# Kernel tuning notes

Measured on AMD Instinct MI355X. Metric: run time of the kernel, lower is better.

The kernel has to match this reference:

```python
import jax, jax.numpy as jnp
import numpy as np

B, S, D = 4, 4096, 128

def setup_inputs() -> dict:
    key = jax.random.key(0)
    kq, kk, kv = jax.random.split(key, 3)
    q = jax.random.normal(kq, (B, S, D), dtype=jnp.float32)
    k = jax.random.normal(kk, (B, S, D), dtype=jnp.float32)
    v = jax.random.normal(kv, (B, S, D), dtype=jnp.float32)
    return {"q": q, "k": k, "v": v}

def reference(q, k, v):
    d_model = q.shape[-1]
    scale = 1.0 / jnp.sqrt(jnp.asarray(d_model, q.dtype))
    # [B, S, S] scores
    scores = jnp.einsum('bqd,bkd->bqk', q, k) * scale
    s = q.shape[1]
    causal = jnp.tril(jnp.ones((s, s), dtype=bool))
    neg_inf = jnp.asarray(-jnp.inf, scores.dtype)
    scores = jnp.where(causal[None, :, :], scores, neg_inf)
    attn = jax.nn.softmax(scores, axis=-1)
    return jnp.einsum('bqk,bkd->bqd', attn, v)
```

## Files before the change

kernel.cpp:

```cpp
#include <hip/hip_runtime.h>


#define B_   4
#define S_   4096
#define D_   128
#define BN   64
#define NT_  64
#define QT_  32
#define RMAX 4
#define BLOB_SHORTS 16384
#define MASKVAL (-1.0e30f)

typedef __attribute__((ext_vector_type(8))) short bf16x8;
typedef __attribute__((ext_vector_type(4))) float f32x4;

__device__ __forceinline__ short f2bf(float x) {
    unsigned u = __builtin_bit_cast(unsigned, x);
    unsigned r = (u + 0x7fffu + ((u >> 16) & 1u)) >> 16;
    return (short)r;
}
__device__ __forceinline__ float ex2(float x) { return __builtin_amdgcn_exp2f(x); }
__device__ __forceinline__ unsigned pkbf(float lo, float hi) {
    return (unsigned)(unsigned short)f2bf(lo) | ((unsigned)(unsigned short)f2bf(hi) << 16);
}
__device__ __forceinline__ void gl_lds16(const short* g, short* l) {
    __builtin_amdgcn_global_load_lds(
        (const __attribute__((address_space(1))) unsigned int*)g,
        (__attribute__((address_space(3))) unsigned int*)l, 16, 0, 0);
}

__global__ __launch_bounds__(256) void prep(const float* __restrict__ Qg,
                                            const float* __restrict__ Kg,
                                            const float* __restrict__ Vg,
                                            short* __restrict__ Qbf,
                                            short* __restrict__ KV)
{
    __shared__ short vt[64][40];
    const int id  = blockIdx.x;
    const int tid = threadIdx.x;
    const float SC = 0.12751740f;

    if (id < 1024) {
        const int b = id & 3, tile = (id >> 2) & 63, q4 = id >> 8;
        const int n = q4 * 16 + (tid >> 4);
        const int G = tid & 15;
        const size_t rowoff = ((size_t)b * S_ + (size_t)tile * 64 + n) * D_ + G * 8;
        short* blob = KV + (size_t)(b * NT_ + tile) * BLOB_SHORTS;
        {
            float4 a = *reinterpret_cast<const float4*>(Qg + rowoff);
            float4 c = *reinterpret_cast<const float4*>(Qg + rowoff + 4);
            bf16x8 v;
            v[0] = f2bf(a.x * SC); v[1] = f2bf(a.y * SC); v[2] = f2bf(a.z * SC); v[3] = f2bf(a.w * SC);
            v[4] = f2bf(c.x * SC); v[5] = f2bf(c.y * SC); v[6] = f2bf(c.z * SC); v[7] = f2bf(c.w * SC);
            *reinterpret_cast<bf16x8*>(Qbf + rowoff) = v;
        }
        {
            float4 a = *reinterpret_cast<const float4*>(Kg + rowoff);
            float4 c = *reinterpret_cast<const float4*>(Kg + rowoff + 4);
            bf16x8 v;
            v[0] = f2bf(a.x); v[1] = f2bf(a.y); v[2] = f2bf(a.z); v[3] = f2bf(a.w);
            v[4] = f2bf(c.x); v[5] = f2bf(c.y); v[6] = f2bf(c.z); v[7] = f2bf(c.w);
            const int p = (G & 8) | ((G & 7) ^ (n & 7));
            *reinterpret_cast<bf16x8*>(blob + n * 128 + p * 8) = v;
        }
    } else {
        const int u = id - 1024;
        const int b = u & 3, tile = (u >> 2) & 63, dq = u >> 8;
        short* blob = KV + (size_t)(b * NT_ + tile) * BLOB_SHORTS;
        {
            const int n = tid >> 2, c8 = tid & 3;
            const size_t off = ((size_t)b * S_ + (size_t)tile * 64 + n) * D_ + dq * 32 + c8 * 8;
            float4 a = *reinterpret_cast<const float4*>(Vg + off);
            float4 c = *reinterpret_cast<const float4*>(Vg + off + 4);
            bf16x8 v;
            v[0] = f2bf(a.x); v[1] = f2bf(a.y); v[2] = f2bf(a.z); v[3] = f2bf(a.w);
            v[4] = f2bf(c.x); v[5] = f2bf(c.y); v[6] = f2bf(c.z); v[7] = f2bf(c.w);
            *reinterpret_cast<bf16x8*>(&vt[n][c8 * 8]) = v;
        }
        __syncthreads();
        {
            const int dl = tid >> 3, G = tid & 7;
            const int d  = dq * 32 + dl;
            bf16x8 g;
#pragma unroll
            for (int i = 0; i < 8; ++i) g[i] = vt[G * 8 + i][dl];
            const int p = G ^ (d & 7);
            *reinterpret_cast<bf16x8*>(blob + 8192 + d * 64 + p * 8) = g;
        }
    }
}

template<bool SPLIT>
__global__ __launch_bounds__(512, 4) void fa_fwd(const short* __restrict__ Qbf,
                                                 const short* __restrict__ KV,
                                                 float* __restrict__ Og,
                                                 float* __restrict__ Op,
                                                 float* __restrict__ Ml,
                                                 int R)
{
    __shared__ short lkv[2][BLOB_SHORTS];

    const int tid  = threadIdx.x;
    const int wv   = tid >> 6;
    const int lane = tid & 63;
    const int m    = lane & 15;
    const int quad = lane >> 4;
    const int m7   = m & 7;

    int batch, t, lo, hi, chunk_id;
    {
        const int id = blockIdx.x;
        batch = id & 3;
        if (SPLIT) {
            int u = id >> 2;
            int tt = u / R;
            int r  = u - tt * R;
            t  = QT_ - 1 - tt;
            const int nk = 2 * t + 2;
            lo = r * nk / R;
            hi = (r + 1) * nk / R;
            chunk_id = (batch * QT_ + t) * R + r;
            if (lo >= hi) return;
        } else {
            t  = QT_ - 1 - (id >> 2);
            lo = 0; hi = 2 * t + 2; chunk_id = 0;
        }
    }

    bf16x8 qf[4];
    {
        const short* qp = Qbf + ((size_t)batch * S_ + (size_t)t * 128 + wv * 16 + m) * D_ + quad * 8;
#pragma unroll
        for (int c = 0; c < 4; ++c)
            qf[c] = *reinterpret_cast<const bf16x8*>(qp + c * 32);
    }

    f32x4 acc[8];
#pragma unroll
    for (int i = 0; i < 8; ++i) acc[i] = (f32x4){0.f, 0.f, 0.f, 0.f};
    float mrun = MASKVAL, lrun = 0.f;

    const size_t tilebase = (size_t)batch * NT_ * BLOB_SHORTS;
#define STAGE(KT, BUF) do {                                                   \
        const short* g_ = KV + tilebase + (size_t)(KT) * BLOB_SHORTS + tid * 8;\
        short* l_ = (BUF) + tid * 8;                                          \
        _Pragma("unroll")                                                     \
        for (int c_ = 0; c_ < 4; ++c_)                                        \
            gl_lds16(g_ + c_ * 4096, l_ + c_ * 4096);                         \
    } while (0)

    STAGE(lo, lkv[0]);

    for (int kt = lo; kt < hi; ++kt) {
        const short* cur = lkv[(kt - lo) & 1];
        short* nxt = lkv[(kt - lo + 1) & 1];
        __syncthreads();
        if (kt + 1 < hi) STAGE(kt + 1, nxt);

        const short* lk = cur;
        const short* lv = cur + 8192;

        f32x4 st[4];
#pragma unroll
        for (int nt = 0; nt < 4; ++nt) st[nt] = (f32x4){0.f, 0.f, 0.f, 0.f};
#pragma unroll
        for (int c = 0; c < 4; ++c) {
            const int p = ((c >> 1) * 8) | ((((c & 1) * 4) | quad) ^ m7);
#pragma unroll
            for (int nt = 0; nt < 4; ++nt) {
                bf16x8 kf = *reinterpret_cast<const bf16x8*>(lk + nt * 2048 + m * 128 + p * 8);
                st[nt] = __builtin_amdgcn_mfma_f32_16x16x32_bf16(kf, qf[c], st[nt], 0, 0, 0);
            }
        }

        if (kt >= 2 * t) {
            const int kbase = (kt - 2 * t) * 64;
            const int qloc  = wv * 16 + m;
#pragma unroll
            for (int nt = 0; nt < 4; ++nt)
#pragma unroll
                for (int r = 0; r < 4; ++r)
                    if (kbase + nt * 16 + quad * 4 + r > qloc) st[nt][r] = MASKVAL;
        }

        float mx = MASKVAL;
#pragma unroll
        for (int nt = 0; nt < 4; ++nt)
#pragma unroll
            for (int r = 0; r < 4; ++r) mx = fmaxf(mx, st[nt][r]);
        mx = fmaxf(mx, __shfl_xor(mx, 16));
        mx = fmaxf(mx, __shfl_xor(mx, 32));
        const float mnew = fmaxf(mrun, mx);
        const float al   = ex2(mrun - mnew);
        mrun = mnew;
        float sum = 0.f;
#pragma unroll
        for (int nt = 0; nt < 4; ++nt)
#pragma unroll
            for (int r = 0; r < 4; ++r) {
                float pv = ex2(st[nt][r] - mnew);
                st[nt][r] = pv;
                sum += pv;
            }
        sum += __shfl_xor(sum, 16);
        sum += __shfl_xor(sum, 32);
        lrun = lrun * al + sum;
#pragma unroll
        for (int r = 0; r < 4; ++r) {
            float alq = __shfl(al, quad * 4 + r);
#pragma unroll
            for (int ct = 0; ct < 8; ++ct) acc[ct][r] *= alq;
        }

        const int srcA = ((quad & 1) << 5) + m;
        const int srcB = srcA + 16;
        const bool loq = quad < 2;
#pragma unroll
        for (int ks = 0; ks < 2; ++ks) {
            unsigned pk0 = pkbf(st[2 * ks][0],     st[2 * ks][1]);
            unsigned pk1 = pkbf(st[2 * ks][2],     st[2 * ks][3]);
            unsigned pk2 = pkbf(st[2 * ks + 1][0], st[2 * ks + 1][1]);
            unsigned pk3 = pkbf(st[2 * ks + 1][2], st[2 * ks + 1][3]);
            unsigned w0a = __shfl((int)pk0, srcA);
            unsigned w0b = __shfl((int)pk2, srcA);
            unsigned w1a = __shfl((int)pk1, srcA);
            unsigned w1b = __shfl((int)pk3, srcA);
            unsigned w2a = __shfl((int)pk0, srcB);
            unsigned w2b = __shfl((int)pk2, srcB);
            unsigned w3a = __shfl((int)pk1, srcB);
            unsigned w3b = __shfl((int)pk3, srcB);
            int4 wi;
            wi.x = (int)(loq ? w0a : w0b);
            wi.y = (int)(loq ? w1a : w1b);
            wi.z = (int)(loq ? w2a : w2b);
            wi.w = (int)(loq ? w3a : w3b);
            bf16x8 pf = __builtin_bit_cast(bf16x8, wi);
            const int p = (ks * 4 + quad) ^ m7;
#pragma unroll
            for (int ct = 0; ct < 8; ++ct) {
                bf16x8 vf = *reinterpret_cast<const bf16x8*>(lv + ct * 1024 + m * 64 + p * 8);
                acc[ct] = __builtin_amdgcn_mfma_f32_16x16x32_bf16(pf, vf, acc[ct], 0, 0, 0);
            }
        }
    }
#undef STAGE

    const int row0 = wv * 16 + quad * 4;
    if (SPLIT) {
        float* ob = Op + (size_t)chunk_id * (128 * D_);
#pragma unroll
        for (int r = 0; r < 4; ++r)
#pragma unroll
            for (int ct = 0; ct < 8; ++ct)
                ob[(row0 + r) * D_ + ct * 16 + m] = acc[ct][r];
        if (lane < 16) {
            float* mlb = Ml + (size_t)chunk_id * (128 * 2) + (wv * 16 + lane) * 2;
            mlb[0] = mrun;
            mlb[1] = lrun;
        }
    } else {
        const float inv = 1.0f / lrun;
        const size_t obase = ((size_t)batch * S_ + (size_t)t * 128 + row0) * D_;
#pragma unroll
        for (int r = 0; r < 4; ++r) {
            float invq = __shfl(inv, quad * 4 + r);
#pragma unroll
            for (int ct = 0; ct < 8; ++ct)
                Og[obase + (size_t)r * D_ + ct * 16 + m] = acc[ct][r] * invq;
        }
    }
}

template<int RR>
__global__ __launch_bounds__(256) void fa_merge(const float* __restrict__ Op,
                                                const float* __restrict__ Ml,
                                                float* __restrict__ Og)
{
    const int x   = blockIdx.x;
    const int btq = x >> 4;
    const int oct = x & 15;
    const int t   = btq & (QT_ - 1);
    const int nk  = 2 * t + 2;
    const int row = oct * 8 + (threadIdx.x >> 5);
    const int cg  = threadIdx.x & 31;
    const size_t cbase = (size_t)btq * RR;

    float mg = MASKVAL;
#pragma unroll
    for (int r = 0; r < RR; ++r) {
        int lo = r * nk / RR, hi = (r + 1) * nk / RR;
        if (lo < hi) mg = fmaxf(mg, Ml[(cbase + r) * (128 * 2) + row * 2]);
    }
    float l = 0.f;
    f32x4 a = (f32x4){0.f, 0.f, 0.f, 0.f};
#pragma unroll
    for (int r = 0; r < RR; ++r) {
        int lo = r * nk / RR, hi = (r + 1) * nk / RR;
        if (lo >= hi) continue;
        float mr = Ml[(cbase + r) * (128 * 2) + row * 2];
        float lr = Ml[(cbase + r) * (128 * 2) + row * 2 + 1];
        float w  = ex2(mr - mg);
        l += lr * w;
        a += w * *reinterpret_cast<const f32x4*>(Op + (cbase + r) * (128 * D_) + row * D_ + cg * 4);
    }
    *reinterpret_cast<f32x4*>(Og + (size_t)btq * (128 * D_) + row * D_ + cg * 4) = a * (1.0f / l);
}

extern "C" void kernel_launch(void* const* d_in, const int* in_sizes, int n_in,
                              void* d_out, int out_size, void* d_ws, size_t ws_size,
                              hipStream_t stream) {
    const float* q = (const float*)d_in[0];
    const float* k = (const float*)d_in[1];
    const float* v = (const float*)d_in[2];
    float* o = (float*)d_out;

    const size_t QBF_BYTES = (size_t)B_ * S_ * D_ * 2;
    const size_t KV_BYTES  = (size_t)B_ * NT_ * BLOB_SHORTS * 2;
    const size_t PREFIX    = QBF_BYTES + KV_BYTES;
    const size_t O_FLOATS  = (size_t)B_ * QT_ * 128 * D_;
    const size_t ML_FLOATS = (size_t)B_ * QT_ * 128 * 2;
    const size_t PER_R     = (O_FLOATS + ML_FLOATS) * sizeof(float);

    char* ws = (char*)d_ws;
    short* Qbf = (short*)ws;
    short* KV  = (short*)(ws + QBF_BYTES);

    int R = 0;
    if (ws_size > PREFIX) {
        R = (int)((ws_size - PREFIX) / PER_R);
        if (R > RMAX) R = RMAX;
    }

    prep<<<dim3(2048), 256, 0, stream>>>(q, k, v, Qbf, KV);

    if (R >= 1) {
        float* Op = (float*)(ws + PREFIX);
        float* Ml = Op + (size_t)R * O_FLOATS;
        fa_fwd<true><<<dim3(B_ * QT_ * R), 512, 0, stream>>>(Qbf, KV, nullptr, Op, Ml, R);
        switch (R) {
            case 1: fa_merge<1><<<dim3(B_ * QT_ * 16), 256, 0, stream>>>(Op, Ml, o); break;
            case 2: fa_merge<2><<<dim3(B_ * QT_ * 16), 256, 0, stream>>>(Op, Ml, o); break;
            case 3: fa_merge<3><<<dim3(B_ * QT_ * 16), 256, 0, stream>>>(Op, Ml, o); break;
            default: fa_merge<4><<<dim3(B_ * QT_ * 16), 256, 0, stream>>>(Op, Ml, o); break;
        }
    } else {
        fa_fwd<false><<<dim3(B_ * QT_), 512, 0, stream>>>(Qbf, KV, o, nullptr, nullptr, 1);
    }
}
```

Before: 123.5 us.

## Switch attention kernel to 32x32x16 MFMA with 4 waves of 32 rows

```diff
diff --git a/kernel.cpp b/kernel.cpp
--- a/kernel.cpp
+++ b/kernel.cpp
@@ -13,6 +13,7 @@
 
 typedef __attribute__((ext_vector_type(8))) short bf16x8;
 typedef __attribute__((ext_vector_type(4))) float f32x4;
+typedef __attribute__((ext_vector_type(16))) float f32x16;
 
 __device__ __forceinline__ short f2bf(float x) {
     unsigned u = __builtin_bit_cast(unsigned, x);
@@ -91,7 +92,7 @@
 }
 
 template<bool SPLIT>
-__global__ __launch_bounds__(512, 4) void fa_fwd(const short* __restrict__ Qbf,
+__global__ __launch_bounds__(256, 2) void fa_fwd(const short* __restrict__ Qbf,
                                                  const short* __restrict__ KV,
                                                  float* __restrict__ Og,
                                                  float* __restrict__ Op,
@@ -103,9 +104,9 @@
     const int tid  = threadIdx.x;
     const int wv   = tid >> 6;
     const int lane = tid & 63;
-    const int m    = lane & 15;
-    const int quad = lane >> 4;
-    const int m7   = m & 7;
+    const int col  = lane & 31;
+    const int half = lane >> 5;
+    const int c7   = col & 7;
 
     int batch, t, lo, hi, chunk_id;
     {
@@ -127,17 +128,19 @@
         }
     }
 
-    bf16x8 qf[4];
+    bf16x8 qf[8];
     {
-        const short* qp = Qbf + ((size_t)batch * S_ + (size_t)t * 128 + wv * 16 + m) * D_ + quad * 8;
-#pragma unroll
-        for (int c = 0; c < 4; ++c)
-            qf[c] = *reinterpret_cast<const bf16x8*>(qp + c * 32);
-    }
-
-    f32x4 acc[8];
-#pragma unroll
-    for (int i = 0; i < 8; ++i) acc[i] = (f32x4){0.f, 0.f, 0.f, 0.f};
+        const short* qp = Qbf + ((size_t)batch * S_ + (size_t)t * 128 + wv * 32 + col) * D_ + half * 8;
+#pragma unroll
+        for (int c = 0; c < 8; ++c)
+            qf[c] = *reinterpret_cast<const bf16x8*>(qp + c * 16);
+    }
+
+    f32x16 acc[4];
+#pragma unroll
+    for (int i = 0; i < 4; ++i)
+#pragma unroll
+        for (int r = 0; r < 16; ++r) acc[i][r] = 0.f;
     float mrun = MASKVAL, lrun = 0.f;
 
     const size_t tilebase = (size_t)batch * NT_ * BLOB_SHORTS;
@@ -145,8 +148,8 @@
         const short* g_ = KV + tilebase + (size_t)(KT) * BLOB_SHORTS + tid * 8;\
         short* l_ = (BUF) + tid * 8;                                          \
         _Pragma("unroll")                                                     \
-        for (int c_ = 0; c_ < 4; ++c_)                                        \
-            gl_lds16(g_ + c_ * 4096, l_ + c_ * 4096);                         \
+        for (int c_ = 0; c_ < 8; ++c_)                                        \
+            gl_lds16(g_ + c_ * 2048, l_ + c_ * 2048);                         \
     } while (0)
 
     STAGE(lo, lkv[0]);
@@ -160,114 +163,124 @@
         const short* lk = cur;
         const short* lv = cur + 8192;
 
-        f32x4 st[4];
-#pragma unroll
-        for (int nt = 0; nt < 4; ++nt) st[nt] = (f32x4){0.f, 0.f, 0.f, 0.f};
-#pragma unroll
-        for (int c = 0; c < 4; ++c) {
-            const int p = ((c >> 1) * 8) | ((((c & 1) * 4) | quad) ^ m7);
-#pragma unroll
-            for (int nt = 0; nt < 4; ++nt) {
-                bf16x8 kf = *reinterpret_cast<const bf16x8*>(lk + nt * 2048 + m * 128 + p * 8);
-                st[nt] = __builtin_amdgcn_mfma_f32_16x16x32_bf16(kf, qf[c], st[nt], 0, 0, 0);
+        f32x16 st[2];
+#pragma unroll
+        for (int i = 0; i < 2; ++i)
+#pragma unroll
+            for (int r = 0; r < 16; ++r) st[i][r] = 0.f;
+#pragma unroll
+        for (int c = 0; c < 8; ++c) {
+            const int G = 2 * c + half;
+            const int p = (G & 8) | ((G & 7) ^ c7);
+#pragma unroll
+            for (int kt32 = 0; kt32 < 2; ++kt32) {
+                const int n = kt32 * 32 + col;
+                bf16x8 kf = *reinterpret_cast<const bf16x8*>(lk + n * 128 + p * 8);
+                st[kt32] = __builtin_amdgcn_mfma_f32_32x32x16_bf16(kf, qf[c], st[kt32], 0, 0, 0);
             }
         }
 
         if (kt >= 2 * t) {
             const int kbase = (kt - 2 * t) * 64;
-            const int qloc  = wv * 16 + m;
-#pragma unroll
-            for (int nt = 0; nt < 4; ++nt)
-#pragma unroll
-                for (int r = 0; r < 4; ++r)
-                    if (kbase + nt * 16 + quad * 4 + r > qloc) st[nt][r] = MASKVAL;
+            const int qloc  = wv * 32 + col;
+#pragma unroll
+            for (int kt32 = 0; kt32 < 2; ++kt32)
+#pragma unroll
+                for (int r = 0; r < 16; ++r) {
+                    const int kl = kt32 * 32 + (r & 3) + 8 * (r >> 2) + 4 * half;
+                    if (kbase + kl > qloc) st[kt32][r] = MASKVAL;
+                }
         }
 
         float mx = MASKVAL;
 #pragma unroll
-        for (int nt = 0; nt < 4; ++nt)
-#pragma unroll
-            for (int r = 0; r < 4; ++r) mx = fmaxf(mx, st[nt][r]);
-        mx = fmaxf(mx, __shfl_xor(mx, 16));
+        for (int i = 0; i < 2; ++i)
+#pragma unroll
+            for (int r = 0; r < 16; ++r) mx = fmaxf(mx, st[i][r]);
         mx = fmaxf(mx, __shfl_xor(mx, 32));
         const float mnew = fmaxf(mrun, mx);
         const float al   = ex2(mrun - mnew);
         mrun = mnew;
         float sum = 0.f;
 #pragma unroll
-        for (int nt = 0; nt < 4; ++nt)
-#pragma unroll
-            for (int r = 0; r < 4; ++r) {
-                float pv = ex2(st[nt][r] - mnew);
-                st[nt][r] = pv;
+        for (int i = 0; i < 2; ++i)
+#pragma unroll
+            for (int r = 0; r < 16; ++r) {
+                float pv = ex2(st[i][r] - mnew);
+                st[i][r] = pv;
                 sum += pv;
             }
-        sum += __shfl_xor(sum, 16);
         sum += __shfl_xor(sum, 32);
         lrun = lrun * al + sum;
 #pragma unroll
-        for (int r = 0; r < 4; ++r) {
-            float alq = __shfl(al, quad * 4 + r);
-#pragma unroll
-            for (int ct = 0; ct < 8; ++ct) acc[ct][r] *= alq;
-        }
-
-        const int srcA = ((quad & 1) << 5) + m;
-        const int srcB = srcA + 16;
-        const bool loq = quad < 2;
-#pragma unroll
-        for (int ks = 0; ks < 2; ++ks) {
-            unsigned pk0 = pkbf(st[2 * ks][0],     st[2 * ks][1]);
-            unsigned pk1 = pkbf(st[2 * ks][2],     st[2 * ks][3]);
-            unsigned pk2 = pkbf(st[2 * ks + 1][0], st[2 * ks + 1][1]);
-            unsigned pk3 = pkbf(st[2 * ks + 1][2], st[2 * ks + 1][3]);
-            unsigned w0a = __shfl((int)pk0, srcA);
-            unsigned w0b = __shfl((int)pk2, srcA);
-            unsigned w1a = __shfl((int)pk1, srcA);
-            unsigned w1b = __shfl((int)pk3, srcA);
-            unsigned w2a = __shfl((int)pk0, srcB);
-            unsigned w2b = __shfl((int)pk2, srcB);
-            unsigned w3a = __shfl((int)pk1, srcB);
-            unsigned w3b = __shfl((int)pk3, srcB);
-            int4 wi;
-            wi.x = (int)(loq ? w0a : w0b);
-            wi.y = (int)(loq ? w1a : w1b);
-            wi.z = (int)(loq ? w2a : w2b);
-            wi.w = (int)(loq ? w3a : w3b);
-            bf16x8 pf = __builtin_bit_cast(bf16x8, wi);
-            const int p = (ks * 4 + quad) ^ m7;
-#pragma unroll
-            for (int ct = 0; ct < 8; ++ct) {
-                bf16x8 vf = *reinterpret_cast<const bf16x8*>(lv + ct * 1024 + m * 64 + p * 8);
-                acc[ct] = __builtin_amdgcn_mfma_f32_16x16x32_bf16(pf, vf, acc[ct], 0, 0, 0);
+        for (int i = 0; i < 4; ++i)
+#pragma unroll
+            for (int r = 0; r < 16; ++r) acc[i][r] *= al;
+
+#pragma unroll
+        for (int kt32 = 0; kt32 < 2; ++kt32) {
+            unsigned pw[4][2];
+#pragma unroll
+            for (int w = 0; w < 4; ++w) {
+                pw[w][0] = pkbf(st[kt32][4 * w],     st[kt32][4 * w + 1]);
+                pw[w][1] = pkbf(st[kt32][4 * w + 2], st[kt32][4 * w + 3]);
+            }
+#pragma unroll
+            for (int s1 = 0; s1 < 2; ++s1) {
+                unsigned snd0 = pw[2 * s1 + 1 - half][0];
+                unsigned snd1 = pw[2 * s1 + 1 - half][1];
+                unsigned rcv0 = __shfl_xor((int)snd0, 32);
+                unsigned rcv1 = __shfl_xor((int)snd1, 32);
+                unsigned own0 = pw[2 * s1 + half][0];
+                unsigned own1 = pw[2 * s1 + half][1];
+                int4 wi;
+                wi.x = (int)(half ? rcv0 : own0);
+                wi.y = (int)(half ? rcv1 : own1);
+                wi.z = (int)(half ? own0 : rcv0);
+                wi.w = (int)(half ? own1 : rcv1);
+                bf16x8 pf = __builtin_bit_cast(bf16x8, wi);
+                const int step = kt32 * 2 + s1;
+                const int G = 2 * step + half;
+                const int p = G ^ c7;
+#pragma unroll
+                for (int dt = 0; dt < 4; ++dt) {
+                    const int d = dt * 32 + col;
+                    bf16x8 vf = *reinterpret_cast<const bf16x8*>(lv + d * 64 + p * 8);
+                    acc[dt] = __builtin_amdgcn_mfma_f32_32x32x16_bf16(vf, pf, acc[dt], 0, 0, 0);
+                }
             }
         }
     }
 #undef STAGE
 
-    const int row0 = wv * 16 + quad * 4;
+    const int qloc = wv * 32 + col;
     if (SPLIT) {
-        float* ob = Op + (size_t)chunk_id * (128 * D_);
-#pragma unroll
-        for (int r = 0; r < 4; ++r)
-#pragma unroll
-            for (int ct = 0; ct < 8; ++ct)
-                ob[(row0 + r) * D_ + ct * 16 + m] = acc[ct][r];
-        if (lane < 16) {
-            float* mlb = Ml + (size_t)chunk_id * (128 * 2) + (wv * 16 + lane) * 2;
+        float* ob = Op + (size_t)chunk_id * (128 * D_) + (size_t)qloc * D_;
+#pragma unroll
+        for (int dt = 0; dt < 4; ++dt)
+#pragma unroll
+            for (int g = 0; g < 4; ++g) {
+                const int d0 = dt * 32 + 8 * g + 4 * half;
+                f32x4 v4 = {acc[dt][4 * g], acc[dt][4 * g + 1], acc[dt][4 * g + 2], acc[dt][4 * g + 3]};
+                *reinterpret_cast<f32x4*>(ob + d0) = v4;
+            }
+        if (half == 0) {
+            float* mlb = Ml + (size_t)chunk_id * (128 * 2) + qloc * 2;
             mlb[0] = mrun;
             mlb[1] = lrun;
         }
     } else {
         const float inv = 1.0f / lrun;
-        const size_t obase = ((size_t)batch * S_ + (size_t)t * 128 + row0) * D_;
-#pragma unroll
-        for (int r = 0; r < 4; ++r) {
-            float invq = __shfl(inv, quad * 4 + r);
-#pragma unroll
-            for (int ct = 0; ct < 8; ++ct)
-                Og[obase + (size_t)r * D_ + ct * 16 + m] = acc[ct][r] * invq;
-        }
+        float* og = Og + ((size_t)batch * S_ + (size_t)t * 128 + qloc) * D_;
+#pragma unroll
+        for (int dt = 0; dt < 4; ++dt)
+#pragma unroll
+            for (int g = 0; g < 4; ++g) {
+                const int d0 = dt * 32 + 8 * g + 4 * half;
+                f32x4 v4 = {acc[dt][4 * g] * inv, acc[dt][4 * g + 1] * inv,
+                            acc[dt][4 * g + 2] * inv, acc[dt][4 * g + 3] * inv};
+                *reinterpret_cast<f32x4*>(og + d0) = v4;
+            }
     }
 }
 
@@ -336,7 +349,7 @@
     if (R >= 1) {
         float* Op = (float*)(ws + PREFIX);
         float* Ml = Op + (size_t)R * O_FLOATS;
-        fa_fwd<true><<<dim3(B_ * QT_ * R), 512, 0, stream>>>(Qbf, KV, nullptr, Op, Ml, R);
+        fa_fwd<true><<<dim3(B_ * QT_ * R), 256, 0, stream>>>(Qbf, KV, nullptr, Op, Ml, R);
         switch (R) {
             case 1: fa_merge<1><<<dim3(B_ * QT_ * 16), 256, 0, stream>>>(Op, Ml, o); break;
             case 2: fa_merge<2><<<dim3(B_ * QT_ * 16), 256, 0, stream>>>(Op, Ml, o); break;
@@ -344,6 +357,6 @@
             default: fa_merge<4><<<dim3(B_ * QT_ * 16), 256, 0, stream>>>(Op, Ml, o); break;
         }
     } else {
-        fa_fwd<false><<<dim3(B_ * QT_), 512, 0, stream>>>(Qbf, KV, o, nullptr, nullptr, 1);
-    }
-}
+        fa_fwd<false><<<dim3(B_ * QT_), 256, 0, stream>>>(Qbf, KV, o, nullptr, nullptr, 1);
+    }
+}
```

Result: no change. 124.9 us (+1.2%).
